# Kernel tuning notes

Measured on AMD Instinct MI355X. Metric: run time of the kernel, lower is better.

## Reference

```python
import jax, jax.numpy as jnp
from jax import lax
import numpy as np

NUM_HEAD = 4
D_MODEL = 160
HEAD_DIM = D_MODEL // NUM_HEAD  # 40
FEAT_DIM = 64
F_SIZE = (128, 128)
B = 4
LN_EPS = 1e-5
LEAKY_SLOPE = 0.01
DN = ('NCHW', 'OIHW', 'NCHW')


def setup_inputs() -> dict:
    key = jax.random.key(0)
    ks = jax.random.split(key, 10)
    pe_len = (F_SIZE[0] // 2) * (F_SIZE[1] // 2) + 1  # 4097
    s = 0.05
    return {
        'x': jax.random.normal(ks[0], (B, FEAT_DIM, F_SIZE[0], F_SIZE[1]), jnp.float32),
        'conv1_w': jax.random.normal(ks[1], (FEAT_DIM, FEAT_DIM, 2, 2), jnp.float32) * s,
        'conv1_b': jax.random.normal(ks[2], (FEAT_DIM,), jnp.float32) * s,
        'conv2_w': jax.random.normal(ks[3], (D_MODEL, FEAT_DIM, 1, 1), jnp.float32) * s,
        'conv2_b': jax.random.normal(ks[4], (D_MODEL,), jnp.float32) * s,
        'pe': jax.random.uniform(ks[5], (pe_len, 1), jnp.float32),
        'wq': jax.random.normal(ks[6], (D_MODEL, D_MODEL), jnp.float32) * s,
        'wk': jax.random.normal(ks[7], (D_MODEL, D_MODEL), jnp.float32) * s,
        'wv': jax.random.normal(ks[8], (D_MODEL, D_MODEL), jnp.float32) * s,
        'ln_w': jnp.ones((D_MODEL,), jnp.float32),
        'ln_b': jnp.zeros((D_MODEL,), jnp.float32),
    }


def reference(x, conv1_w, conv1_b, conv2_w, conv2_b, pe, wq, wk, wv, ln_w, ln_b):
    b = x.shape[0]
    # patch embed: stride-2 conv -> 1x1 conv -> LeakyReLU
    f = lax.conv_general_dilated(x, conv1_w, (2, 2), 'VALID', dimension_numbers=DN)
    f = f + conv1_b[None, :, None, None]
    f = lax.conv_general_dilated(f, conv2_w, (1, 1), 'VALID', dimension_numbers=DN)
    f = f + conv2_b[None, :, None, None]
    f = jnp.where(f >= 0, f, LEAKY_SLOPE * f)
    _, c, h, w = f.shape  # [b, 160, 64, 64]
    f = f.reshape(b, c, h * w).transpose(0, 2, 1)  # [b, s, d]
    # pad one extra token at end of sequence, add positional encoding [s+1, 1]
    f = jnp.pad(f, ((0, 0), (0, 1), (0, 0))) + pe  # [b, s+1, d]
    s1 = f.shape[1]
    # torch Linear (no bias): y = x @ W.T
    q = (f @ wq.T).reshape(b, s1, NUM_HEAD, HEAD_DIM).transpose(0, 2, 1, 3)
    k = (f @ wk.T).reshape(b, s1, NUM_HEAD, HEAD_DIM).transpose(0, 2, 1, 3)
    v = (f @ wv.T).reshape(b, s1, NUM_HEAD, HEAD_DIM).transpose(0, 2, 1, 3)
    score = jnp.einsum('bhqd,bhkd->bhqk', q, k) / jnp.sqrt(jnp.float32(HEAD_DIM))
    score = jax.nn.softmax(score, axis=-1)
    att = jnp.einsum('bhqk,bhkd->bhqd', score, v)  # [b, h, s+1, hd]
    cat = att.transpose(0, 2, 1, 3).reshape(b, s1, D_MODEL)
    feat = cat[:, :-1, :]  # drop padded token -> [b, s, d]
    # residual LayerNorm: LN(feat) + feat
    mu = jnp.mean(feat, axis=-1, keepdims=True)
    var = jnp.mean(jnp.square(feat - mu), axis=-1, keepdims=True)
    ln = (feat - mu) / jnp.sqrt(var + LN_EPS) * ln_w + ln_b
    feat = ln + feat
    feat = feat.transpose(0, 2, 1).reshape(b, D_MODEL, h, w)  # [b, 160, 64, 64]
    feat = jnp.repeat(jnp.repeat(feat, 2, axis=2), 2, axis=3)
    return feat
```

## Files before the change

### kernel.cpp

```cpp
#include <hip/hip_runtime.h>

typedef _Float16 f16;
typedef _Float16 half2v __attribute__((ext_vector_type(2)));
typedef _Float16 half4v __attribute__((ext_vector_type(4)));
typedef _Float16 half8 __attribute__((ext_vector_type(8)));
typedef float f32x4 __attribute__((ext_vector_type(4)));
typedef unsigned u32x4 __attribute__((ext_vector_type(4)));

#define MFMA16(a, b, c) __builtin_amdgcn_mfma_f32_16x16x32_f16((a), (b), (c), 0, 0, 0)

__device__ __forceinline__ unsigned pk2(float a, float b) {
  return __builtin_bit_cast(unsigned, __builtin_amdgcn_cvt_pkrtz(a, b));
}

__device__ __forceinline__ void plswap_pair(unsigned& a, unsigned& b) {
  asm("s_nop 1\n\t"
      "v_permlane32_swap_b32 %0, %1\n\t"
      "v_permlane16_swap_b32 %0, %1"
      : "+v"(a), "+v"(b));
}


__global__ __launch_bounds__(256) void k_convqkv(
    const float* __restrict__ x, const float* __restrict__ w1, const float* __restrict__ b1,
    const float* __restrict__ w2, const float* __restrict__ b2, const float* __restrict__ pe,
    const float* __restrict__ wq, const float* __restrict__ wk, const float* __restrict__ wv,
    f16* __restrict__ q_h, f16* __restrict__ k_h, f16* __restrict__ vt_h,
    float* __restrict__ kmaxp) {
  __shared__ __attribute__((aligned(16))) char smem[112192];
  f16* fT   = (f16*)smem;
  f16* xh   = (f16*)(smem + 21504);
  f16* wT   = (f16*)(smem + 21504);
  float* red = (float*)(smem + 48384);
  f16* w1h  = (f16*)(smem + 55360);
  f16* c1t  = (f16*)(smem + 55360);
  f16* Lv   = (f16*)(smem + 55360);
  float* red160 = (float*)(smem + 64576);
  f16* w2h  = (f16*)(smem + 89152);

  const float c1l = 0.15811388300841898f * 1.4426950408889634f;

  int y = blockIdx.x, b = blockIdx.y;
  int t = threadIdx.x, lane = t & 63, wv4 = t >> 6, quad = lane >> 4, col = lane & 15;
  int s0 = y * 64;

  const float* xb = x + (b * 64) * 16384 + (2 * y) * 128;
#pragma unroll
  for (int it = 0; it < 32; ++it) {
    int flat = t + it * 256;
    int pos = flat & 63, r = (flat >> 6) & 1, ci = flat >> 7;
    float2 v = *(const float2*)(xb + ci * 16384 + r * 128 + 2 * pos);
    *(unsigned*)(xh + pos * 264 + ci * 4 + r * 2) = pk2(v.x, v.y);
  }
#pragma unroll
  for (int it = 0; it < 16; ++it) {
    int i4 = t + it * 256;
    int co = i4 >> 6, q4 = (i4 & 63) * 4;
    f32x4 v = *(const f32x4*)(w1 + co * 256 + q4);
    uint2 u = {pk2(v[0], v[1]), pk2(v[2], v[3])};
    *(uint2*)(w1h + co * 264 + q4) = u;
  }
#pragma unroll
  for (int it = 0; it < 10; ++it) {
    int i4 = t + it * 256;
    int c2 = i4 >> 4, q4 = (i4 & 15) * 4;
    f32x4 v = *(const f32x4*)(w2 + c2 * 64 + q4);
    uint2 u = {pk2(v[0], v[1]), pk2(v[2], v[3])};
    *(uint2*)(w2h + c2 * 72 + q4) = u;
  }
  __syncthreads();

  float b1v[4];
#pragma unroll
  for (int r = 0; r < 4; ++r) b1v[r] = b1[wv4 * 16 + quad * 4 + r];
  f32x4 acc1[4];
#pragma unroll
  for (int nt = 0; nt < 4; ++nt)
#pragma unroll
    for (int r = 0; r < 4; ++r) acc1[nt][r] = b1v[r];
#pragma unroll
  for (int kk = 0; kk < 8; ++kk) {
    half8 a = *(half8*)(w1h + (wv4 * 16 + col) * 264 + kk * 32 + quad * 8);
#pragma unroll
    for (int nt = 0; nt < 4; ++nt) {
      half8 bfr = *(half8*)(xh + (nt * 16 + col) * 264 + kk * 32 + quad * 8);
      acc1[nt] = MFMA16(a, bfr, acc1[nt]);
    }
  }
  __syncthreads();
#pragma unroll
  for (int nt = 0; nt < 4; ++nt) {
    uint2 u = {pk2(acc1[nt][0], acc1[nt][1]), pk2(acc1[nt][2], acc1[nt][3])};
    *(uint2*)(c1t + (nt * 16 + col) * 72 + wv4 * 16 + quad * 4) = u;
  }
  __syncthreads();

  f32x4 acc2[10];
#pragma unroll
  for (int mt = 0; mt < 10; ++mt)
#pragma unroll
    for (int r = 0; r < 4; ++r) acc2[mt][r] = b2[mt * 16 + quad * 4 + r];
  half8 bb0 = *(half8*)(c1t + (wv4 * 16 + col) * 72 + quad * 8);
  half8 bb1 = *(half8*)(c1t + (wv4 * 16 + col) * 72 + 32 + quad * 8);
#pragma unroll
  for (int mt = 0; mt < 10; ++mt) {
    half8 a0 = *(half8*)(w2h + (mt * 16 + col) * 72 + quad * 8);
    half8 a1 = *(half8*)(w2h + (mt * 16 + col) * 72 + 32 + quad * 8);
    acc2[mt] = MFMA16(a0, bb0, acc2[mt]);
    acc2[mt] = MFMA16(a1, bb1, acc2[mt]);
  }
  float pes = pe[s0 + wv4 * 16 + col];
#pragma unroll
  for (int mt = 0; mt < 10; ++mt) {
    float p[4];
#pragma unroll
    for (int r = 0; r < 4; ++r) {
      float v = acc2[mt][r];
      v = (v >= 0.f) ? v : 0.01f * v;
      p[r] = v + pes;
    }
    uint2 u = {pk2(p[0], p[1]), pk2(p[2], p[3])};
    *(uint2*)(fT + (wv4 * 16 + col) * 168 + mt * 16 + quad * 4) = u;
  }
  __syncthreads();

  half8 af[5];
  int rowA = wv4 * 16 + col;
#pragma unroll
  for (int kk = 0; kk < 5; ++kk)
    af[kk] = *(half8*)(fT + rowA * 168 + kk * 32 + quad * 8);

  float ks0[4], ks1[4];
#pragma unroll
  for (int r = 0; r < 4; ++r) { ks0[r] = 0.f; ks1[r] = 0.f; }

  for (int kind = 0; kind < 3; ++kind) {
    const float* wsp = (kind == 0) ? wq : (kind == 1 ? wk : wv);
    for (int hf = 0; hf < 2; ++hf) {
      __syncthreads();
      for (int c = t; c < 1600; c += 256) {
        int row = c / 20, seg = c - row * 20;
        const float* src = wsp + (hf * 80 + row) * 160 + seg * 8;
        f32x4 va = *(const f32x4*)src;
        f32x4 vb = *(const f32x4*)(src + 4);
        uint4 u = {pk2(va[0], va[1]), pk2(va[2], va[3]), pk2(vb[0], vb[1]), pk2(vb[2], vb[3])};
        *(uint4*)(wT + row * 168 + seg * 8) = u;
      }
      __syncthreads();
#pragma unroll
      for (int n0 = 0; n0 < 5; ++n0) {
        f32x4 acc; acc[0] = 0.f; acc[1] = 0.f; acc[2] = 0.f; acc[3] = 0.f;
        int rowB = n0 * 16 + col;
#pragma unroll
        for (int kk = 0; kk < 5; ++kk) {
          half8 bf = *(half8*)(wT + rowB * 168 + kk * 32 + quad * 8);
          acc = MFMA16(af[kk], bf, acc);
        }
        int o = (hf * 5 + n0) * 16 + col;
        int hh = o / 40, d = o - hh * 40;
        int bh = b * 4 + hh;
        if (kind == 1) {
          bool kidx = (n0 * 16 + col) >= 40;
#pragma unroll
          for (int r = 0; r < 4; ++r) {
            float z = acc[r] * acc[r];
            ks0[r] += kidx ? 0.f : z;
            ks1[r] += kidx ? z : 0.f;
          }
        }
        if (kind == 2) {
          half4v hv;
#pragma unroll
          for (int r = 0; r < 4; ++r) hv[r] = (f16)acc[r];
          *(half4v*)(Lv + (n0 * 16 + col) * 72 + wv4 * 16 + quad * 4) = hv;
        } else {
#pragma unroll
          for (int r = 0; r < 4; ++r) {
            int s = s0 + wv4 * 16 + quad * 4 + r;
            if (kind == 0)      q_h[((size_t)bh * 4097 + s) * 40 + d] = (f16)(acc[r] * c1l);
            else                k_h[((size_t)bh * 4160 + s) * 40 + d] = (f16)acc[r];
          }
        }
      }
      if (kind == 1) {
        float m0 = 0.f, m1 = 0.f;
#pragma unroll
        for (int r = 0; r < 4; ++r) {
          float v0 = ks0[r], v1 = ks1[r];
          v0 += __shfl_xor(v0, 1); v0 += __shfl_xor(v0, 2);
          v0 += __shfl_xor(v0, 4); v0 += __shfl_xor(v0, 8);
          v1 += __shfl_xor(v1, 1); v1 += __shfl_xor(v1, 2);
          v1 += __shfl_xor(v1, 4); v1 += __shfl_xor(v1, 8);
          m0 = fmaxf(m0, v0); m1 = fmaxf(m1, v1);
          ks0[r] = 0.f; ks1[r] = 0.f;
        }
        m0 = fmaxf(m0, __shfl_xor(m0, 16)); m0 = fmaxf(m0, __shfl_xor(m0, 32));
        m1 = fmaxf(m1, __shfl_xor(m1, 16)); m1 = fmaxf(m1, __shfl_xor(m1, 32));
        if (lane == 0) { red[wv4 * 4 + hf * 2] = m0; red[wv4 * 4 + hf * 2 + 1] = m1; }
      }
      if (kind == 2) {
        __syncthreads();
        for (int c = t; c < 640; c += 256) {
          int row = c >> 3, seg = c & 7;
          int o = hf * 80 + row, hh = o / 40, d = o - hh * 40;
          *(uint4*)(vt_h + ((size_t)(b * 4 + hh) * 40 + d) * 4160 + s0 + seg * 8) =
              *(const uint4*)(Lv + row * 72 + seg * 8);
        }
      }
    }
  }
  __syncthreads();
  if (t < 4) {
    float m = fmaxf(fmaxf(red[t], red[4 + t]), fmaxf(red[8 + t], red[12 + t]));
    kmaxp[(b * 4 + t) * 65 + y] = m;
  }

  if (y == 63) {
    float pe4 = pe[4096];
    if (t < 160) {
      int hh = t / 40, d = t - hh * 40, bh = b * 4 + hh;
#pragma unroll
      for (int kind = 0; kind < 3; ++kind) {
        const float* wsp = (kind == 0) ? wq : (kind == 1 ? wk : wv);
        const float* wr = wsp + t * 160;
        float rs = 0.f;
#pragma unroll
        for (int c4 = 0; c4 < 40; ++c4) {
          f32x4 v = *(const f32x4*)(wr + c4 * 4);
          rs += v[0] + v[1] + v[2] + v[3];
        }
        float val = pe4 * rs;
        if (kind == 0)      q_h[((size_t)bh * 4097 + 4096) * 40 + d] = (f16)(val * c1l);
        else if (kind == 1) { k_h[((size_t)bh * 4160 + 4096) * 40 + d] = (f16)val;
                              red160[t] = val * val; }
        else                vt_h[((size_t)bh * 40 + d) * 4160 + 4096] = (f16)val;
      }
    }
    __syncthreads();
    if (t < 4) {
      float s = 0.f;
#pragma unroll
      for (int j = 0; j < 40; ++j) s += red160[t * 40 + j];
      kmaxp[(b * 4 + t) * 65 + 64] = s;
    }
  }
}

__global__ __launch_bounds__(256, 4) void k_attn(
    const f16* __restrict__ q_h, const f16* __restrict__ k_h,
    const f16* __restrict__ vt_h, const float* __restrict__ kmaxp,
    float* __restrict__ pacc) {
  __shared__ __attribute__((aligned(16))) f16 Ks[2][64 * 40];
  __shared__ __attribute__((aligned(16))) f16 Vs[2][40 * 72];
  __shared__ __attribute__((aligned(16))) f16 Ones[8];
  __shared__ __attribute__((aligned(16))) f16 Zro[8];
  __shared__ __attribute__((aligned(16))) float red4[4];

  int qt = blockIdx.x, bh = blockIdx.y, ks = blockIdx.z;
  int qbase = qt * 128;
  int t = threadIdx.x, lane = t & 63, wv = t >> 6, quad = lane >> 4, col = lane & 15;
  int gbase = ks * 33;
  int nIter = 33 - ks;

  if (t < 8) { Zro[t] = (f16)0; Ones[t] = (f16)1; }
  {
    float vm = (t < 65) ? kmaxp[bh * 65 + t] : 0.f;
#pragma unroll
    for (int d = 1; d < 64; d <<= 1) vm = fmaxf(vm, __shfl_xor(vm, d));
    if (lane == 0) red4[wv] = vm;
  }

  const f16* khb = k_h + ((size_t)bh * 4160 + gbase * 64) * 40;
  const f16* vtb = vt_h + (size_t)bh * 40 * 4160;
  int vrow = t >> 3, vseg = t & 7;
  uint4 rka = *(const uint4*)(khb + t * 8);
  uint4 rkb = {0, 0, 0, 0}, rvb = {0, 0, 0, 0};
  if (t < 64) rkb = *(const uint4*)(khb + (256 + t) * 8);
  uint4 rva = *(const uint4*)(vtb + vrow * 4160 + gbase * 64 + vseg * 8);
  if (t < 64) rvb = *(const uint4*)(vtb + (32 + vrow) * 4160 + gbase * 64 + vseg * 8);

  half8 zero8;
#pragma unroll
  for (int j = 0; j < 8; ++j) zero8[j] = (f16)0;

  half8 bq[2][2], q32[2];
#pragma unroll
  for (int nt = 0; nt < 2; ++nt) {
    const f16* qr = q_h + ((size_t)bh * 4097 + qbase + wv * 32 + nt * 16 + col) * 40;
    bq[nt][0] = *(const half8*)(qr + quad * 8);
    q32[nt] = *(const half8*)(qr + 32);
  }
  __syncthreads();

  float mk = fmaxf(fmaxf(red4[0], red4[1]), fmaxf(red4[2], red4[3]));

#pragma unroll
  for (int nt = 0; nt < 2; ++nt) {
    float s = 0.f;
#pragma unroll
    for (int j = 0; j < 8; ++j) {
      float a0 = (float)bq[nt][0][j];
      s += a0 * a0;
    }
    s += __shfl_xor(s, 16);
    s += __shfl_xor(s, 32);
#pragma unroll
    for (int j = 0; j < 8; ++j) {
      float a1 = (float)q32[nt][j];
      s += a1 * a1;
    }
    float mfl = sqrtf(s * mk) - 14.0f;
    half8 e = zero8;
    e[0] = (f16)(-mfl);
    bq[nt][1] = (quad == 0) ? q32[nt] : ((quad == 1) ? e : zero8);
  }

  f32x4 o_[2][3];
#pragma unroll
  for (int a = 0; a < 2; ++a)
#pragma unroll
    for (int b2 = 0; b2 < 3; ++b2)
#pragma unroll
      for (int r = 0; r < 4; ++r) o_[a][b2][r] = 0.f;

  for (int kt = 0; kt < nIter; ++kt) {
    int bsel = kt & 1;
    int g = gbase + kt;
    *(uint4*)(&Ks[bsel][t * 8]) = rka;
    if (t < 64) *(uint4*)(&Ks[bsel][(256 + t) * 8]) = rkb;
    *(uint4*)(&Vs[bsel][vrow * 72 + vseg * 8]) = rva;
    if (t < 64) *(uint4*)(&Vs[bsel][(32 + vrow) * 72 + vseg * 8]) = rvb;
    if (kt + 1 < nIter) {
      const f16* kn = khb + (size_t)(kt + 1) * 2560;
      int k0n = (g + 1) << 6;
      rka = *(const uint4*)(kn + t * 8);
      if (t < 64) rkb = *(const uint4*)(kn + (256 + t) * 8);
      rva = *(const uint4*)(vtb + vrow * 4160 + k0n + vseg * 8);
      if (t < 64) rvb = *(const uint4*)(vtb + (32 + vrow) * 4160 + k0n + vseg * 8);
    }
    __syncthreads();

    bool lastt = (g == 64);

    f32x4 acc[4][2];
#pragma unroll
    for (int mt = 0; mt < 4; ++mt) {
      int row = mt * 16 + col;
      half8 ak0 = *(half8*)(&Ks[bsel][row * 40 + quad * 8]);
      const f16* pa1 = (quad == 0) ? &Ks[bsel][row * 40 + 32]
                                   : ((quad == 1) ? Ones : Zro);
      half8 ak1 = *(half8*)pa1;
#pragma unroll
      for (int nt = 0; nt < 2; ++nt) {
        f32x4 a; a[0] = 0.f; a[1] = 0.f; a[2] = 0.f; a[3] = 0.f;
        a = MFMA16(ak0, bq[nt][0], a);
        a = MFMA16(ak1, bq[nt][1], a);
        acc[mt][nt] = a;
      }
    }

    half8 pa[2][2];
#pragma unroll
    for (int kk2 = 0; kk2 < 2; ++kk2)
#pragma unroll
      for (int nt = 0; nt < 2; ++nt) {
        float p0[4], p1[4];
#pragma unroll
        for (int r = 0; r < 4; ++r) {
          p0[r] = __builtin_amdgcn_exp2f(acc[kk2 * 2][nt][r]);
          p1[r] = __builtin_amdgcn_exp2f(acc[kk2 * 2 + 1][nt][r]);
        }
        if (__builtin_expect(lastt, 0)) {
#pragma unroll
          for (int r = 0; r < 4; ++r) {
            p0[r] = (kk2 == 0 && (quad * 4 + r) == 0) ? p0[r] : 0.f;
            p1[r] = 0.f;
          }
        }
        unsigned sr[4];
        sr[0] = pk2(p0[0], p0[1]);
        sr[1] = pk2(p0[2], p0[3]);
        sr[2] = pk2(p1[0], p1[1]);
        sr[3] = pk2(p1[2], p1[3]);
        plswap_pair(sr[0], sr[2]);
        plswap_pair(sr[1], sr[3]);
        u32x4 uu; uu[0] = sr[0]; uu[1] = sr[1]; uu[2] = sr[2]; uu[3] = sr[3];
        pa[kk2][nt] = __builtin_bit_cast(half8, uu);
      }

#pragma unroll
    for (int kk2 = 0; kk2 < 2; ++kk2)
#pragma unroll
      for (int nv = 0; nv < 3; ++nv) {
        int d = nv * 16 + col;
        const f16* vp = (d < 40) ? &Vs[bsel][d * 72 + kk2 * 32 + quad * 8]
                                 : ((d == 40) ? Ones : Zro);
        half8 bv = *(half8*)vp;
        o_[0][nv] = MFMA16(pa[kk2][0], bv, o_[0][nv]);
        o_[1][nv] = MFMA16(pa[kk2][1], bv, o_[1][nv]);
      }
  }

  float* pb = pacc + (size_t)(ks * 16 + bh) * 4096 * 48;
#pragma unroll
  for (int mtq = 0; mtq < 2; ++mtq)
#pragma unroll
    for (int nv = 0; nv < 3; ++nv)
#pragma unroll
      for (int r = 0; r < 4; ++r) {
        int q = qbase + wv * 32 + mtq * 16 + quad * 4 + r;
        pb[(size_t)q * 48 + nv * 16 + col] = o_[mtq][nv][r];
      }
}

__global__ __launch_bounds__(256) void k_ln_out(
    const float* __restrict__ pacc, const float* __restrict__ lnw,
    const float* __restrict__ lnb, float* __restrict__ out) {
  __shared__ float g[32 * 164];
  __shared__ float linv[32 * 4];
  int y = blockIdx.x, b = blockIdx.y, z = blockIdx.z, t = threadIdx.x;
  const size_t P1 = (size_t)16 * 4096 * 48;
  int w0 = z * 32;
  if (t < 128) {
    int row = t >> 2, h = t & 3;
    size_t i0 = ((size_t)(b * 4 + h) * 4096 + y * 64 + w0 + row) * 48 + 40;
    linv[row * 4 + h] = 1.f / (pacc[i0] + pacc[P1 + i0]);
  }
  __syncthreads();
#pragma unroll
  for (int it = 0; it < 5; ++it) {
    int flat = t + it * 256;
    int row = flat / 40, dq = flat - row * 40;
    int h = dq / 10, d = (dq - h * 10) * 4;
    size_t idx = ((size_t)(b * 4 + h) * 4096 + y * 64 + w0 + row) * 48 + d;
    f32x4 v0 = *(const f32x4*)(pacc + idx);
    f32x4 v1 = *(const f32x4*)(pacc + P1 + idx);
    float li = linv[row * 4 + h];
    f32x4 gv;
#pragma unroll
    for (int j = 0; j < 4; ++j) gv[j] = (v0[j] + v1[j]) * li;
    *(f32x4*)(g + row * 164 + h * 40 + d) = gv;
  }
  __syncthreads();
  int row = t >> 3, part = t & 7;
  float* gr = g + row * 164 + part * 20;
  float s1 = 0.f, s2 = 0.f;
#pragma unroll
  for (int j4 = 0; j4 < 5; ++j4) {
    f32x4 v = *(f32x4*)(gr + j4 * 4);
#pragma unroll
    for (int j = 0; j < 4; ++j) { s1 += v[j]; s2 += v[j] * v[j]; }
  }
  s1 += __shfl_xor(s1, 1); s1 += __shfl_xor(s1, 2); s1 += __shfl_xor(s1, 4);
  s2 += __shfl_xor(s2, 1); s2 += __shfl_xor(s2, 2); s2 += __shfl_xor(s2, 4);
  float mu = s1 * (1.f / 160.f);
  float var = s2 * (1.f / 160.f) - mu * mu;
  float inv = rsqrtf(var + 1e-5f);
  const float* lw = lnw + part * 20;
  const float* lb = lnb + part * 20;
#pragma unroll
  for (int j = 0; j < 20; ++j) {
    float v = gr[j];
    gr[j] = (v - mu) * inv * lw[j] + lb[j] + v;
  }
  __syncthreads();
  int Yo = t >> 7, xp = t & 63, cpar = (t >> 6) & 1;
  int rl = xp >> 1;
  float* ob = out + (2 * y + Yo) * 128 + z * 64 + xp;
  for (int c = cpar; c < 160; c += 2)
    ob[(size_t)(b * 160 + c) * 16384] = g[rl * 164 + c];
}

extern "C" void kernel_launch(void* const* d_in, const int* in_sizes, int n_in,
                              void* d_out, int out_size, void* d_ws, size_t ws_size,
                              hipStream_t stream) {
  const float* x   = (const float*)d_in[0];
  const float* w1  = (const float*)d_in[1];
  const float* b1  = (const float*)d_in[2];
  const float* w2  = (const float*)d_in[3];
  const float* b2  = (const float*)d_in[4];
  const float* pe  = (const float*)d_in[5];
  const float* wq  = (const float*)d_in[6];
  const float* wk  = (const float*)d_in[7];
  const float* wvp = (const float*)d_in[8];
  const float* lnw = (const float*)d_in[9];
  const float* lnb = (const float*)d_in[10];
  float* out = (float*)d_out;

  char* p = (char*)d_ws;
  f16* q_h   = (f16*)p;   p += (size_t)16 * 4097 * 40 * 2;
  f16* k_h   = (f16*)p;   p += (size_t)16 * 4160 * 40 * 2;
  f16* vt_h  = (f16*)p;   p += (size_t)16 * 40 * 4160 * 2;
  float* pacc = (float*)p; p += (size_t)2 * 16 * 4096 * 48 * 4;
  float* kmaxp = (float*)p; p += 16 * 65 * 4;

  k_convqkv<<<dim3(64, 4), 256, 0, stream>>>(x, w1, b1, w2, b2, pe, wq, wk, wvp,
                                             q_h, k_h, vt_h, kmaxp);
  k_attn<<<dim3(32, 16, 2), 256, 0, stream>>>(q_h, k_h, vt_h, kmaxp, pacc);
  k_ln_out<<<dim3(64, 4, 2), 256, 0, stream>>>(pacc, lnw, lnb, out);
}
```

Measured before the change: 201.2 us.

## Split fused conv+QKV kernel into separate conv, QKV, and key-norm kernels

The monolithic conv+QKV kernel (256 blocks, large LDS) is split into several launches. A weight-prep kernel converts the projection weights to f16, the conv kernel writes the f16 embedding to global memory, a QKV kernel runs 768 blocks (one per projection kind), and a separate kernel computes the per-slot key-norm maxima. The LayerNorm/upsample kernel is also split into twice as many smaller blocks. The aim is more parallelism and less serialized work per block, at the cost of extra launches and an extra global round-trip for the embedding.

```diff
diff --git a/kernel.cpp b/kernel.cpp
--- a/kernel.cpp
+++ b/kernel.cpp
@@ -21,20 +21,28 @@
 }
 
 
-__global__ __launch_bounds__(256) void k_convqkv(
+__global__ __launch_bounds__(256) void k_prep(
+    const float* __restrict__ wq, const float* __restrict__ wk,
+    const float* __restrict__ wv, f16* __restrict__ wf) {
+  int kind = blockIdx.y;
+  const float* src = (kind == 0) ? wq : (kind == 1 ? wk : wv);
+  int i4 = blockIdx.x * 256 + threadIdx.x;
+  f32x4 v = *(const f32x4*)(src + i4 * 4);
+  uint2 u = {pk2(v[0], v[1]), pk2(v[2], v[3])};
+  *(uint2*)(wf + (size_t)kind * 25600 + i4 * 4) = u;
+}
+
+__global__ __launch_bounds__(256) void k_conv(
     const float* __restrict__ x, const float* __restrict__ w1, const float* __restrict__ b1,
     const float* __restrict__ w2, const float* __restrict__ b2, const float* __restrict__ pe,
     const float* __restrict__ wq, const float* __restrict__ wk, const float* __restrict__ wv,
-    f16* __restrict__ q_h, f16* __restrict__ k_h, f16* __restrict__ vt_h,
-    float* __restrict__ kmaxp) {
+    f16* __restrict__ fh, f16* __restrict__ q_h, f16* __restrict__ k_h,
+    f16* __restrict__ vt_h, float* __restrict__ kmaxp) {
   __shared__ __attribute__((aligned(16))) char smem[112192];
   f16* fT   = (f16*)smem;
   f16* xh   = (f16*)(smem + 21504);
-  f16* wT   = (f16*)(smem + 21504);
-  float* red = (float*)(smem + 48384);
   f16* w1h  = (f16*)(smem + 55360);
   f16* c1t  = (f16*)(smem + 55360);
-  f16* Lv   = (f16*)(smem + 55360);
   float* red160 = (float*)(smem + 64576);
   f16* w2h  = (f16*)(smem + 89152);
 
@@ -124,95 +132,12 @@
   }
   __syncthreads();
 
-  half8 af[5];
-  int rowA = wv4 * 16 + col;
-#pragma unroll
-  for (int kk = 0; kk < 5; ++kk)
-    af[kk] = *(half8*)(fT + rowA * 168 + kk * 32 + quad * 8);
-
-  float ks0[4], ks1[4];
-#pragma unroll
-  for (int r = 0; r < 4; ++r) { ks0[r] = 0.f; ks1[r] = 0.f; }
-
-  for (int kind = 0; kind < 3; ++kind) {
-    const float* wsp = (kind == 0) ? wq : (kind == 1 ? wk : wv);
-    for (int hf = 0; hf < 2; ++hf) {
-      __syncthreads();
-      for (int c = t; c < 1600; c += 256) {
-        int row = c / 20, seg = c - row * 20;
-        const float* src = wsp + (hf * 80 + row) * 160 + seg * 8;
-        f32x4 va = *(const f32x4*)src;
-        f32x4 vb = *(const f32x4*)(src + 4);
-        uint4 u = {pk2(va[0], va[1]), pk2(va[2], va[3]), pk2(vb[0], vb[1]), pk2(vb[2], vb[3])};
-        *(uint4*)(wT + row * 168 + seg * 8) = u;
-      }
-      __syncthreads();
-#pragma unroll
-      for (int n0 = 0; n0 < 5; ++n0) {
-        f32x4 acc; acc[0] = 0.f; acc[1] = 0.f; acc[2] = 0.f; acc[3] = 0.f;
-        int rowB = n0 * 16 + col;
-#pragma unroll
-        for (int kk = 0; kk < 5; ++kk) {
-          half8 bf = *(half8*)(wT + rowB * 168 + kk * 32 + quad * 8);
-          acc = MFMA16(af[kk], bf, acc);
-        }
-        int o = (hf * 5 + n0) * 16 + col;
-        int hh = o / 40, d = o - hh * 40;
-        int bh = b * 4 + hh;
-        if (kind == 1) {
-          bool kidx = (n0 * 16 + col) >= 40;
-#pragma unroll
-          for (int r = 0; r < 4; ++r) {
-            float z = acc[r] * acc[r];
-            ks0[r] += kidx ? 0.f : z;
-            ks1[r] += kidx ? z : 0.f;
-          }
-        }
-        if (kind == 2) {
-          half4v hv;
-#pragma unroll
-          for (int r = 0; r < 4; ++r) hv[r] = (f16)acc[r];
-          *(half4v*)(Lv + (n0 * 16 + col) * 72 + wv4 * 16 + quad * 4) = hv;
-        } else {
-#pragma unroll
-          for (int r = 0; r < 4; ++r) {
-            int s = s0 + wv4 * 16 + quad * 4 + r;
-            if (kind == 0)      q_h[((size_t)bh * 4097 + s) * 40 + d] = (f16)(acc[r] * c1l);
-            else                k_h[((size_t)bh * 4160 + s) * 40 + d] = (f16)acc[r];
-          }
-        }
-      }
-      if (kind == 1) {
-        float m0 = 0.f, m1 = 0.f;
-#pragma unroll
-        for (int r = 0; r < 4; ++r) {
-          float v0 = ks0[r], v1 = ks1[r];
-          v0 += __shfl_xor(v0, 1); v0 += __shfl_xor(v0, 2);
-          v0 += __shfl_xor(v0, 4); v0 += __shfl_xor(v0, 8);
-          v1 += __shfl_xor(v1, 1); v1 += __shfl_xor(v1, 2);
-          v1 += __shfl_xor(v1, 4); v1 += __shfl_xor(v1, 8);
-          m0 = fmaxf(m0, v0); m1 = fmaxf(m1, v1);
-          ks0[r] = 0.f; ks1[r] = 0.f;
-        }
-        m0 = fmaxf(m0, __shfl_xor(m0, 16)); m0 = fmaxf(m0, __shfl_xor(m0, 32));
-        m1 = fmaxf(m1, __shfl_xor(m1, 16)); m1 = fmaxf(m1, __shfl_xor(m1, 32));
-        if (lane == 0) { red[wv4 * 4 + hf * 2] = m0; red[wv4 * 4 + hf * 2 + 1] = m1; }
-      }
-      if (kind == 2) {
-        __syncthreads();
-        for (int c = t; c < 640; c += 256) {
-          int row = c >> 3, seg = c & 7;
-          int o = hf * 80 + row, hh = o / 40, d = o - hh * 40;
-          *(uint4*)(vt_h + ((size_t)(b * 4 + hh) * 40 + d) * 4160 + s0 + seg * 8) =
-              *(const uint4*)(Lv + row * 72 + seg * 8);
-        }
-      }
-    }
-  }
-  __syncthreads();
-  if (t < 4) {
-    float m = fmaxf(fmaxf(red[t], red[4 + t]), fmaxf(red[8 + t], red[12 + t]));
-    kmaxp[(b * 4 + t) * 65 + y] = m;
+#pragma unroll
+  for (int it = 0; it < 5; ++it) {
+    int flat = t + it * 256;
+    int row = flat / 20, seg = flat - row * 20;
+    *(uint4*)(fh + ((size_t)b * 4096 + s0 + row) * 160 + seg * 8) =
+        *(const uint4*)(fT + row * 168 + seg * 8);
   }
 
   if (y == 63) {
@@ -244,6 +169,80 @@
       kmaxp[(b * 4 + t) * 65 + 64] = s;
     }
   }
+}
+
+__global__ __launch_bounds__(256) void k_qkv(
+    const f16* __restrict__ fh, const f16* __restrict__ wf,
+    f16* __restrict__ q_h, f16* __restrict__ k_h, f16* __restrict__ vt_h) {
+  __shared__ __attribute__((aligned(16))) f16 Lv[160 * 72];
+  int y = blockIdx.x, b = blockIdx.y, kind = blockIdx.z;
+  int t = threadIdx.x, lane = t & 63, wvv = t >> 6, quad = lane >> 4, col = lane & 15;
+  int s0 = y * 64;
+  const float c1l = 0.15811388300841898f * 1.4426950408889634f;
+  const f16* wk_ = wf + (size_t)kind * 25600;
+
+  half8 af[5];
+  int rowA = wvv * 16 + col;
+#pragma unroll
+  for (int kk = 0; kk < 5; ++kk)
+    af[kk] = *(const half8*)(fh + ((size_t)b * 4096 + s0 + rowA) * 160 + kk * 32 + quad * 8);
+
+#pragma unroll
+  for (int n0 = 0; n0 < 10; ++n0) {
+    f32x4 acc; acc[0] = 0.f; acc[1] = 0.f; acc[2] = 0.f; acc[3] = 0.f;
+    int rowB = n0 * 16 + col;
+#pragma unroll
+    for (int kk = 0; kk < 5; ++kk) {
+      half8 bf = *(const half8*)(wk_ + rowB * 160 + kk * 32 + quad * 8);
+      acc = MFMA16(af[kk], bf, acc);
+    }
+    int o = n0 * 16 + col;
+    int hh = o / 40, d = o - hh * 40;
+    int bh = b * 4 + hh;
+    if (kind == 2) {
+      half4v hv;
+#pragma unroll
+      for (int r = 0; r < 4; ++r) hv[r] = (f16)acc[r];
+      *(half4v*)(Lv + o * 72 + wvv * 16 + quad * 4) = hv;
+    } else {
+#pragma unroll
+      for (int r = 0; r < 4; ++r) {
+        int s = s0 + wvv * 16 + quad * 4 + r;
+        if (kind == 0) q_h[((size_t)bh * 4097 + s) * 40 + d] = (f16)(acc[r] * c1l);
+        else           k_h[((size_t)bh * 4160 + s) * 40 + d] = (f16)acc[r];
+      }
+    }
+  }
+  if (kind == 2) {
+    __syncthreads();
+#pragma unroll
+    for (int it = 0; it < 5; ++it) {
+      int c = t + it * 256;
+      int row = c >> 3, seg = c & 7;
+      int hh = row / 40, d = row - hh * 40;
+      *(uint4*)(vt_h + ((size_t)(b * 4 + hh) * 40 + d) * 4160 + s0 + seg * 8) =
+          *(const uint4*)(Lv + row * 72 + seg * 8);
+    }
+  }
+}
+
+__global__ __launch_bounds__(256) void k_sq(
+    const f16* __restrict__ k_h, float* __restrict__ kmaxp) {
+  int t = threadIdx.x, lane = t & 63, wvv = t >> 6;
+  int slot = blockIdx.x * 4 + wvv;
+  int bh = blockIdx.y;
+  int s = slot * 64 + lane;
+  const f16* kr = k_h + ((size_t)bh * 4160 + s) * 40;
+  float sum = 0.f;
+#pragma unroll
+  for (int i = 0; i < 5; ++i) {
+    half8 v = *(const half8*)(kr + i * 8);
+#pragma unroll
+    for (int j = 0; j < 8; ++j) { float xv = (float)v[j]; sum += xv * xv; }
+  }
+#pragma unroll
+  for (int d = 1; d < 64; d <<= 1) sum = fmaxf(sum, __shfl_xor(sum, d));
+  if (lane == 0) kmaxp[bh * 65 + slot] = sum;
 }
 
 __global__ __launch_bounds__(256, 4) void k_attn(
@@ -416,58 +415,58 @@
 __global__ __launch_bounds__(256) void k_ln_out(
     const float* __restrict__ pacc, const float* __restrict__ lnw,
     const float* __restrict__ lnb, float* __restrict__ out) {
-  __shared__ float g[32 * 164];
-  __shared__ float linv[32 * 4];
+  __shared__ float g[16 * 164];
+  __shared__ float linv[16 * 4];
   int y = blockIdx.x, b = blockIdx.y, z = blockIdx.z, t = threadIdx.x;
   const size_t P1 = (size_t)16 * 4096 * 48;
-  int w0 = z * 32;
-  if (t < 128) {
+  int w0 = z * 16;
+  if (t < 64) {
     int row = t >> 2, h = t & 3;
     size_t i0 = ((size_t)(b * 4 + h) * 4096 + y * 64 + w0 + row) * 48 + 40;
     linv[row * 4 + h] = 1.f / (pacc[i0] + pacc[P1 + i0]);
   }
   __syncthreads();
 #pragma unroll
-  for (int it = 0; it < 5; ++it) {
+  for (int it = 0; it < 3; ++it) {
     int flat = t + it * 256;
-    int row = flat / 40, dq = flat - row * 40;
-    int h = dq / 10, d = (dq - h * 10) * 4;
-    size_t idx = ((size_t)(b * 4 + h) * 4096 + y * 64 + w0 + row) * 48 + d;
-    f32x4 v0 = *(const f32x4*)(pacc + idx);
-    f32x4 v1 = *(const f32x4*)(pacc + P1 + idx);
-    float li = linv[row * 4 + h];
-    f32x4 gv;
-#pragma unroll
-    for (int j = 0; j < 4; ++j) gv[j] = (v0[j] + v1[j]) * li;
-    *(f32x4*)(g + row * 164 + h * 40 + d) = gv;
-  }
-  __syncthreads();
-  int row = t >> 3, part = t & 7;
-  float* gr = g + row * 164 + part * 20;
+    if (flat < 640) {
+      int row = flat / 40, dq = flat - row * 40;
+      int h = dq / 10, d = (dq - h * 10) * 4;
+      size_t idx = ((size_t)(b * 4 + h) * 4096 + y * 64 + w0 + row) * 48 + d;
+      f32x4 v0 = *(const f32x4*)(pacc + idx);
+      f32x4 v1 = *(const f32x4*)(pacc + P1 + idx);
+      float li = linv[row * 4 + h];
+      f32x4 gv;
+#pragma unroll
+      for (int j = 0; j < 4; ++j) gv[j] = (v0[j] + v1[j]) * li;
+      *(f32x4*)(g + row * 164 + h * 40 + d) = gv;
+    }
+  }
+  __syncthreads();
+  int row = t >> 4, part = t & 15;
+  float* gr = g + row * 164 + part * 10;
   float s1 = 0.f, s2 = 0.f;
 #pragma unroll
-  for (int j4 = 0; j4 < 5; ++j4) {
-    f32x4 v = *(f32x4*)(gr + j4 * 4);
-#pragma unroll
-    for (int j = 0; j < 4; ++j) { s1 += v[j]; s2 += v[j] * v[j]; }
-  }
-  s1 += __shfl_xor(s1, 1); s1 += __shfl_xor(s1, 2); s1 += __shfl_xor(s1, 4);
-  s2 += __shfl_xor(s2, 1); s2 += __shfl_xor(s2, 2); s2 += __shfl_xor(s2, 4);
+  for (int j = 0; j < 10; ++j) { float v = gr[j]; s1 += v; s2 += v * v; }
+  s1 += __shfl_xor(s1, 1); s1 += __shfl_xor(s1, 2);
+  s1 += __shfl_xor(s1, 4); s1 += __shfl_xor(s1, 8);
+  s2 += __shfl_xor(s2, 1); s2 += __shfl_xor(s2, 2);
+  s2 += __shfl_xor(s2, 4); s2 += __shfl_xor(s2, 8);
   float mu = s1 * (1.f / 160.f);
   float var = s2 * (1.f / 160.f) - mu * mu;
   float inv = rsqrtf(var + 1e-5f);
-  const float* lw = lnw + part * 20;
-  const float* lb = lnb + part * 20;
-#pragma unroll
-  for (int j = 0; j < 20; ++j) {
+  const float* lw = lnw + part * 10;
+  const float* lb = lnb + part * 10;
+#pragma unroll
+  for (int j = 0; j < 10; ++j) {
     float v = gr[j];
     gr[j] = (v - mu) * inv * lw[j] + lb[j] + v;
   }
   __syncthreads();
-  int Yo = t >> 7, xp = t & 63, cpar = (t >> 6) & 1;
+  int Yo = t >> 7, rem = t & 127, xp = rem & 31, cpar = rem >> 5;
   int rl = xp >> 1;
-  float* ob = out + (2 * y + Yo) * 128 + z * 64 + xp;
-  for (int c = cpar; c < 160; c += 2)
+  float* ob = out + (2 * y + Yo) * 128 + z * 32 + xp;
+  for (int c = cpar; c < 160; c += 4)
     ob[(size_t)(b * 160 + c) * 16384] = g[rl * 164 + c];
 }
 
@@ -493,9 +492,14 @@
   f16* vt_h  = (f16*)p;   p += (size_t)16 * 40 * 4160 * 2;
   float* pacc = (float*)p; p += (size_t)2 * 16 * 4096 * 48 * 4;
   float* kmaxp = (float*)p; p += 16 * 65 * 4;
-
-  k_convqkv<<<dim3(64, 4), 256, 0, stream>>>(x, w1, b1, w2, b2, pe, wq, wk, wvp,
-                                             q_h, k_h, vt_h, kmaxp);
+  f16* fh    = (f16*)p;   p += (size_t)4 * 4096 * 160 * 2;
+  f16* wf    = (f16*)p;   p += (size_t)3 * 160 * 160 * 2;
+
+  k_prep<<<dim3(25, 3), 256, 0, stream>>>(wq, wk, wvp, wf);
+  k_conv<<<dim3(64, 4), 256, 0, stream>>>(x, w1, b1, w2, b2, pe, wq, wk, wvp,
+                                          fh, q_h, k_h, vt_h, kmaxp);
+  k_qkv<<<dim3(64, 4, 3), 256, 0, stream>>>(fh, wf, q_h, k_h, vt_h);
+  k_sq<<<dim3(16, 16), 256, 0, stream>>>(k_h, kmaxp);
   k_attn<<<dim3(32, 16, 2), 256, 0, stream>>>(q_h, k_h, vt_h, kmaxp, pacc);
-  k_ln_out<<<dim3(64, 4, 2), 256, 0, stream>>>(pacc, lnw, lnb, out);
-}
+  k_ln_out<<<dim3(64, 4, 4), 256, 0, stream>>>(pacc, lnw, lnb, out);
+}
```

Measured after the change: 201.5 us. Within noise of the previous version (+0.2%).
